# Kernel tuning notes

Measured on AMD Instinct MI355X. Metric: run time of the kernel, lower is better.

## Reference

```python
import jax, jax.numpy as jnp
import numpy as np

IMAGE_SIZE = 256
NEAR = 0.1
FAR = 100.0
EPS = 1e-3
BACKGROUND = jnp.array([0.0, 0.0, 0.0], dtype=jnp.float32)
CHUNK = 64  # faces processed per scan step (keeps [B,CHUNK,3,P] intermediate ~100MB)


def setup_inputs() -> dict:
    key = jax.random.key(0)
    k1, k2, k3, k4 = jax.random.split(key, 4)
    B, F, T = 2, 4096, 4
    # small triangles in NDC with z in (near, far)
    centers = jax.random.uniform(k1, (B, F, 1, 2), minval=-1.0, maxval=1.0)
    offsets = 0.15 * jax.random.normal(k2, (B, F, 3, 2))
    xy = centers + offsets
    z = jax.random.uniform(k3, (B, F, 1, 1), minval=1.0, maxval=20.0) \
        + 0.1 * jax.random.normal(k4, (B, F, 3, 1))
    faces = jnp.concatenate([xy, z], axis=-1).astype(jnp.float32)  # [B,F,3,3]
    textures = jax.random.uniform(jax.random.fold_in(key, 7), (B, F, T, T, T, 3),
                                  dtype=jnp.float32)
    return {"faces": faces, "textures": textures}


def _pixel_grid(is_):
    c = (2.0 * jnp.arange(is_, dtype=jnp.float32) + 1.0 - is_) / is_
    # kernel iterates rows top->bottom with y flipped (y up in NDC)
    yp, xp = jnp.meshgrid(-c, c, indexing="ij")  # [H,W]
    return xp.reshape(-1), yp.reshape(-1)  # [P]


def _raster_chunk(fchunk, xp, yp, near, far):
    # fchunk: [B,C,3verts,3coords]; xp,yp: [P]
    x = fchunk[..., 0]
    y = fchunk[..., 1]
    z = fchunk[..., 2]  # [B,C,3]
    x0, x1, x2 = x[..., 0:1], x[..., 1:2], x[..., 2:3]
    y0, y1, y2 = y[..., 0:1], y[..., 1:2], y[..., 2:3]

    # inside test: pixel on the CCW side of all 3 edges (back faces culled)
    def edge(ya, xa, yb, xb):
        return (yp - ya) * (xb - xa) - (xp - xa) * (yb - ya)  # [B,C,P]
    inside = (edge(y0, x0, y1, x1) >= 0) & (edge(y1, x1, y2, x2) >= 0) \
             & (edge(y2, x2, y0, x0) >= 0)

    # inverse of [[x0,y0,1],[x1,y1,1],[x2,y2,1]] via adjugate (as in CUDA kernel)
    x0s, x1s, x2s = x[..., 0], x[..., 1], x[..., 2]
    y0s, y1s, y2s = y[..., 0], y[..., 1], y[..., 2]
    det = x2s * (y0s - y1s) + x0s * (y1s - y2s) + x1s * (y2s - y0s)
    det = jnp.where(det >= 0, jnp.maximum(det, 1e-10), jnp.minimum(det, -1e-10))
    inv = jnp.stack([
        jnp.stack([y1s - y2s, x2s - x1s, x1s * y2s - x2s * y1s], -1),
        jnp.stack([y2s - y0s, x0s - x2s, x2s * y0s - x0s * y2s], -1),
        jnp.stack([y0s - y1s, x1s - x0s, x0s * y1s - x1s * y0s], -1),
    ], -2) / det[..., None, None]  # [B,C,3,3]

    # barycentric weights per pixel: [B,C,3,P]
    w = inv[..., 0, None] * xp + inv[..., 1, None] * yp + inv[..., 2, None]
    w = jnp.clip(w, 0.0, 1.0)
    w = w / jnp.maximum(w.sum(axis=2, keepdims=True), 1e-10)

    # perspective-correct depth: 1/zp = sum_k w_k / z_k
    inv_zp = (w / z[..., None]).sum(axis=2)  # [B,C,P]
    zp = 1.0 / jnp.maximum(inv_zp, 1e-10)
    valid = inside & (zp > near) & (zp < far)
    zp = jnp.where(valid, zp, far)
    return zp, jnp.moveaxis(w, 2, 3)  # zp:[B,C,P], w:[B,C,P,3]


def _rasterize_maps(faces, image_size, near, far):
    B, F = faces.shape[:2]
    P = image_size * image_size
    xp, yp = _pixel_grid(image_size)
    n_chunks = F // CHUNK
    fch = faces.reshape(B, n_chunks, CHUNK, 3, 3).transpose(1, 0, 2, 3, 4)
    ids = jnp.arange(F, dtype=jnp.int32).reshape(n_chunks, CHUNK)
    init = (jnp.full((B, P), far, jnp.float32),        # best depth (z-buffer)
            jnp.full((B, P), -1, jnp.int32),            # best face index
            jnp.zeros((B, P, 3), jnp.float32))          # best barycentric weights

    def step(carry, inp):
        bz, bf, bw = carry
        fchunk, idc = inp
        zp, w = _raster_chunk(fchunk, xp, yp, near, far)
        am = jnp.argmin(zp, axis=1)  # [B,P] nearest face within chunk
        zmin = jnp.take_along_axis(zp, am[:, None, :], axis=1)[:, 0]          # [B,P]
        wsel = jnp.take_along_axis(w, am[:, None, :, None], axis=1)[:, 0]     # [B,P,3]
        fsel = idc[am]                                                        # [B,P]
        upd = zmin < bz
        return (jnp.where(upd, zmin, bz),
                jnp.where(upd, fsel, bf),
                jnp.where(upd[..., None], wsel, bw)), None

    (bz, bf, bw), _ = jax.lax.scan(jax.checkpoint(step), init, (fch, ids))
    return bf, bw, bz  # face_index_map, weight_map, depth_map (flat pixels)


def _forward(faces, textures):
    B, F = faces.shape[:2]
    T = textures.shape[2]
    is_ = IMAGE_SIZE
    P = is_ * is_
    fidx, w, zp = _rasterize_maps(faces, is_, NEAR, FAR)
    mask = fidx >= 0
    fi = jnp.maximum(fidx, 0)

    # per-pixel vertex depths of hit face: [B,P,3]
    faces_z = faces[..., 2]
    fz = jax.vmap(lambda a, i: a[i])(faces_z, fi)

    # texture cube coords with perspective correction (as in CUDA kernel)
    tif = jnp.clip(w * (T - 1) * (zp[..., None] / fz), 0.0, T - 1 - EPS)
    lo = jnp.floor(tif).astype(jnp.int32)
    frac = tif - lo

    tex_flat = textures.reshape(B, F, T * T * T, 3)
    rgb = jnp.zeros((B, P, 3), jnp.float32)
    for pn in range(8):  # trilinear blend over 8 cube corners
        bits = [(pn >> k) & 1 for k in range(3)]
        idx = lo + jnp.array(bits, jnp.int32)
        wc = jnp.ones_like(frac[..., 0])
        for k in range(3):
            wc = wc * (frac[..., k] if bits[k] else (1.0 - frac[..., k]))
        lin = (idx[..., 0] * T + idx[..., 1]) * T + idx[..., 2]
        texel = jax.vmap(lambda tf, f, l: tf[f, l])(tex_flat, fi, lin)  # [B,P,3]
        rgb = rgb + wc[..., None] * texel

    rgb = jnp.where(mask[..., None], rgb, BACKGROUND)
    alpha = mask.astype(jnp.float32)
    return (rgb.reshape(B, is_, is_, 3),
            alpha.reshape(B, is_, is_),
            zp.reshape(B, is_, is_))


def reference(faces, textures):
    return _forward(faces, textures)
```

## Files before the change

### kernel.cpp

```cpp
#include <hip/hip_runtime.h>

#define IS 256
#define FNUM 4096
#define BATCH 2
#define NSPLIT 16
#define FSPLIT (FNUM / NSPLIT)
#define FAR_ 100.0f
#define NEAR_ 0.1f


__global__ __launch_bounds__(256, 8) void raster_kernel(
    const float* __restrict__ faces, unsigned int* __restrict__ keys)
{
#pragma clang fp contract(off)
  __shared__ float rec[256 * 12];
  __shared__ int cnt[4];

  const int tid = threadIdx.x;
  const int wid = tid >> 6, lane = tid & 63;
  const int z = blockIdx.z;
  const int b = z >> 4;
  const int split = z & 15;

  const int qx = tid & 15, qy = tid >> 4;
  const int col0 = blockIdx.x * 32 + qx * 2;
  const int row0 = blockIdx.y * 32 + qy * 2;

  const float xpA = (2.0f * (float)col0 + 1.0f - 256.0f) * (1.0f / 256.0f);
  const float xpB = (2.0f * (float)(col0 + 1) + 1.0f - 256.0f) * (1.0f / 256.0f);
  const float ypA = -((2.0f * (float)row0 + 1.0f - 256.0f) * (1.0f / 256.0f));
  const float ypB = -((2.0f * (float)(row0 + 1) + 1.0f - 256.0f) * (1.0f / 256.0f));

  const float txmin = (2.0f * (float)(blockIdx.x * 32) + 1.0f - 256.0f) * (1.0f / 256.0f) - 1e-3f;
  const float txmax = (2.0f * (float)(blockIdx.x * 32 + 31) + 1.0f - 256.0f) * (1.0f / 256.0f) + 1e-3f;
  const float tymax = -((2.0f * (float)(blockIdx.y * 32) + 1.0f - 256.0f) * (1.0f / 256.0f)) + 1e-3f;
  const float tymin = -((2.0f * (float)(blockIdx.y * 32 + 31) + 1.0f - 256.0f) * (1.0f / 256.0f)) - 1e-3f;

  const int f = split * FSPLIT + tid;
  const float* fp = faces + ((size_t)b * FNUM + f) * 9;
  const float x0 = fp[0], y0 = fp[1], z0 = fp[2];
  const float x1 = fp[3], y1 = fp[4], z1 = fp[5];
  const float x2 = fp[6], y2 = fp[7], z2 = fp[8];

  const float det = x2 * (y0 - y1) + x0 * (y1 - y2) + x1 * (y2 - y0);
  const float minx = fminf(fminf(x0, x1), x2), maxx = fmaxf(fmaxf(x0, x1), x2);
  const float miny = fminf(fminf(y0, y1), y2), maxy = fmaxf(fmaxf(y0, y1), y2);
  const bool keep = (det >= -1e-5f) &&
                    (minx <= txmax) && (maxx >= txmin) &&
                    (miny <= tymax) && (maxy >= tymin);

  const unsigned long long m = __ballot(keep);
  if (lane == 0) cnt[wid] = __popcll(m);
  __syncthreads();
  const int total = cnt[0] + cnt[1] + cnt[2] + cnt[3];
  if (keep) {
    int base = 0;
    for (int w = 0; w < wid; ++w) base += cnt[w];
    const int pos = base + __popcll(m & ((1ull << lane) - 1ull));
    const float cd = (det >= 0.0f) ? fmaxf(det, 1e-10f) : fminf(det, -1e-10f);
    const float rdet = __builtin_amdgcn_rcpf(cd);
    const float u0 = __builtin_amdgcn_rcpf(z0) * rdet;
    const float u1 = __builtin_amdgcn_rcpf(z1) * rdet;
    const float u2 = __builtin_amdgcn_rcpf(z2) * rdet;
    float4* r4 = (float4*)&rec[pos * 12];
    r4[0] = make_float4(x0, y0, x1, y1);
    r4[1] = make_float4(x2, y2, u0, u1);
    r4[2] = make_float4(u2, __int_as_float(f), 0.0f, 0.0f);
  }
  __syncthreads();

  unsigned int kAA = ~0u, kAB = ~0u, kBA = ~0u, kBB = ~0u;
  for (int i = 0; i < total; ++i) {
    const float4 r0 = ((const float4*)rec)[i * 3 + 0];
    const float4 r1 = ((const float4*)rec)[i * 3 + 1];
    const float4 r2 = ((const float4*)rec)[i * 3 + 2];
    const float fx0 = r0.x, fy0 = r0.y, fx1 = r0.z, fy1 = r0.w;
    const float fx2 = r1.x, fy2 = r1.y, u0 = r1.z, u1 = r1.w;
    const float u2 = r2.x;
    const unsigned int fid = (unsigned int)__float_as_int(r2.y);

    const float t01x = fx1 - fx0, t01y = fy1 - fy0;
    const float t12x = fx2 - fx1, t12y = fy2 - fy1;
    const float t20x = fx0 - fx2, t20y = fy0 - fy2;

    const float a01A = (ypA - fy0) * t01x, a01B = (ypB - fy0) * t01x;
    const float b01A = (xpA - fx0) * t01y, b01B = (xpB - fx0) * t01y;
    const float a12A = (ypA - fy1) * t12x, a12B = (ypB - fy1) * t12x;
    const float b12A = (xpA - fx1) * t12y, b12B = (xpB - fx1) * t12y;
    const float a20A = (ypA - fy2) * t20x, a20B = (ypB - fy2) * t20x;
    const float b20A = (xpA - fx2) * t20y, b20B = (xpB - fx2) * t20y;

#define PX(KK, AR, AC)                                                        \
    {                                                                         \
      const float e01 = a01##AR - b01##AC;                                    \
      const float e12 = a12##AR - b12##AC;                                    \
      const float e20 = a20##AR - b20##AC;                                    \
      const bool inside = fminf(fminf(e01, e12), e20) >= 0.0f;                \
      const float izp = fmaf(e12, u0, fmaf(e20, u1, e01 * u2));               \
      const float zp = __builtin_amdgcn_rcpf(izp);                            \
      const bool valid = inside && (izp > 0.01f) && (izp < 10.0f);            \
      const unsigned int key =                                                \
          valid ? ((__float_as_uint(zp) & 0xFFFFF000u) | fid) : ~0u;          \
      KK = (key < KK) ? key : KK;                                             \
    }
    PX(kAA, A, A) PX(kAB, A, B) PX(kBA, B, A) PX(kBB, B, B)
#undef PX
  }

  const int tbase = z * 65536 + ((int)blockIdx.y * 8 + (int)blockIdx.x) * 1024;
  const int ly = qy * 2, lx = qx * 2;
  keys[tbase + ly * 32 + lx]           = kAA;
  keys[tbase + ly * 32 + lx + 1]       = kAB;
  keys[tbase + (ly + 1) * 32 + lx]     = kBA;
  keys[tbase + (ly + 1) * 32 + lx + 1] = kBB;
}

__global__ __launch_bounds__(256) void resolve_kernel(
    const float* __restrict__ faces, const float* __restrict__ tex,
    const unsigned int* __restrict__ keys,
    float* __restrict__ out_rgb, float* __restrict__ out_alpha,
    float* __restrict__ out_z)
{
#pragma clang fp contract(off)
  const int p = blockIdx.x * 256 + threadIdx.x;
  const int b = p >> 16;
  const int pi = p & 65535;
  const int row = pi >> 8, col = pi & 255;
  const int tidx = ((row >> 5) * 8 + (col >> 5)) * 1024 + (row & 31) * 32 + (col & 31);

  unsigned int key = ~0u;
  for (int s = 0; s < NSPLIT; ++s) {
    const unsigned int k = keys[(b * NSPLIT + s) * 65536 + tidx];
    key = (k < key) ? k : key;
  }

  if (key == ~0u) {
    out_rgb[(size_t)p * 3 + 0] = 0.0f;
    out_rgb[(size_t)p * 3 + 1] = 0.0f;
    out_rgb[(size_t)p * 3 + 2] = 0.0f;
    out_alpha[p] = 0.0f;
    out_z[p] = FAR_;
    return;
  }

  const int fid = (int)(key & 0xFFFu);
  const float xp = (2.0f * (float)col + 1.0f - 256.0f) * (1.0f / 256.0f);
  const float yp = -((2.0f * (float)row + 1.0f - 256.0f) * (1.0f / 256.0f));

  const float* fp = faces + ((size_t)b * FNUM + fid) * 9;
  const float x0 = fp[0], y0 = fp[1], z0 = fp[2];
  const float x1 = fp[3], y1 = fp[4], z1 = fp[5];
  const float x2 = fp[6], y2 = fp[7], z2 = fp[8];

  const float det = x2 * (y0 - y1) + x0 * (y1 - y2) + x1 * (y2 - y0);
  const float cd = (det >= 0.0f) ? fmaxf(det, 1e-10f) : fminf(det, -1e-10f);
  const float rdet = __builtin_amdgcn_rcpf(cd);
  const float rz0 = __builtin_amdgcn_rcpf(z0);
  const float rz1 = __builtin_amdgcn_rcpf(z1);
  const float rz2 = __builtin_amdgcn_rcpf(z2);

  const float e01 = (yp - y0) * (x1 - x0) - (xp - x0) * (y1 - y0);
  const float e12 = (yp - y1) * (x2 - x1) - (xp - x1) * (y2 - y1);
  const float e20 = (yp - y2) * (x0 - x2) - (xp - x2) * (y0 - y2);

  float c0 = fminf(fmaxf(e12 * rdet, 0.0f), 1.0f);
  float c1 = fminf(fmaxf(e20 * rdet, 0.0f), 1.0f);
  float c2 = fminf(fmaxf(e01 * rdet, 0.0f), 1.0f);
  const float s = fmaxf((c0 + c1) + c2, 1e-10f);
  const float rs = __builtin_amdgcn_rcpf(s);
  const float w0 = c0 * rs, w1 = c1 * rs, w2 = c2 * rs;
  const float izp = (w0 * rz0 + w1 * rz1) + w2 * rz2;
  const float zp = __builtin_amdgcn_rcpf(fmaxf(izp, 1e-10f));

  const float t0 = fminf(fmaxf((w0 * 3.0f) * (zp * rz0), 0.0f), 2.999f);
  const float t1 = fminf(fmaxf((w1 * 3.0f) * (zp * rz1), 0.0f), 2.999f);
  const float t2 = fminf(fmaxf((w2 * 3.0f) * (zp * rz2), 0.0f), 2.999f);
  const float l0 = floorf(t0), l1 = floorf(t1), l2 = floorf(t2);
  const int i0 = (int)l0, i1 = (int)l1, i2 = (int)l2;
  const float fr0 = t0 - l0, fr1 = t1 - l1, fr2 = t2 - l2;

  const float* tb = tex + ((size_t)b * FNUM + fid) * 192;
  float rr = 0.f, rg = 0.f, rb = 0.f;
  for (int pn = 0; pn < 8; ++pn) {
    const int b0 = pn & 1, b1 = (pn >> 1) & 1, b2 = (pn >> 2) & 1;
    const float c0w = b0 ? fr0 : (1.0f - fr0);
    const float c1w = b1 ? fr1 : (1.0f - fr1);
    const float c2w = b2 ? fr2 : (1.0f - fr2);
    const float wc = (c0w * c1w) * c2w;
    const int lin = ((i0 + b0) * 4 + (i1 + b1)) * 4 + (i2 + b2);
    const float* tp = tb + lin * 3;
    rr = rr + wc * tp[0];
    rg = rg + wc * tp[1];
    rb = rb + wc * tp[2];
  }

  out_rgb[(size_t)p * 3 + 0] = rr;
  out_rgb[(size_t)p * 3 + 1] = rg;
  out_rgb[(size_t)p * 3 + 2] = rb;
  out_alpha[p] = 1.0f;
  out_z[p] = zp;
}

extern "C" void kernel_launch(void* const* d_in, const int* in_sizes, int n_in,
                              void* d_out, int out_size, void* d_ws, size_t ws_size,
                              hipStream_t stream) {
  const float* faces = (const float*)d_in[0];
  const float* tex   = (const float*)d_in[1];
  float* out = (float*)d_out;
  float* out_rgb   = out;
  float* out_alpha = out + 393216;
  float* out_z     = out + 393216 + 131072;

  unsigned int* keys = (unsigned int*)d_ws;

  dim3 gridA(IS / 32, IS / 32, BATCH * NSPLIT);
  hipLaunchKernelGGL(raster_kernel, gridA, dim3(256), 0, stream, faces, keys);

  dim3 gridC((BATCH * IS * IS) / 256, 1, 1);
  hipLaunchKernelGGL(resolve_kernel, gridC, dim3(256), 0, stream,
                     faces, tex, keys, out_rgb, out_alpha, out_z);
}
```

Measured before the change: 76.60 us.

## Merge split depth keys with atomicMin and vectorize resolve texture loads

The raster kernel now combines its per-split depth keys into one per-pixel buffer with atomicMin, skipping empty pixels. This replaces the 16 partial key buffers and the 16-way reduction in the resolve kernel, cutting global traffic substantially. The depth key is built from the bit-inverted inverse depth, which drops one reciprocal per pixel test. The resolve kernel also loads face data and pairs of texels as packed vectors and restructures the trilinear weights. The trade-offs are an extra memset on the stream and atomic contention, and the key quantization now applies to 1/z rather than z, which can change tie-breaking.

Result: no change. 75.50 us (-1.4%).

```diff
diff --git a/kernel.cpp b/kernel.cpp
--- a/kernel.cpp
+++ b/kernel.cpp
@@ -97,23 +97,24 @@
       const float e20 = a20##AR - b20##AC;                                    \
       const bool inside = fminf(fminf(e01, e12), e20) >= 0.0f;                \
       const float izp = fmaf(e12, u0, fmaf(e20, u1, e01 * u2));               \
-      const float zp = __builtin_amdgcn_rcpf(izp);                            \
       const bool valid = inside && (izp > 0.01f) && (izp < 10.0f);            \
       const unsigned int key =                                                \
-          valid ? ((__float_as_uint(zp) & 0xFFFFF000u) | fid) : ~0u;          \
+          valid ? ((~__float_as_uint(izp)) & 0xFFFFF000u) | fid : ~0u;        \
       KK = (key < KK) ? key : KK;                                             \
     }
     PX(kAA, A, A) PX(kAB, A, B) PX(kBA, B, A) PX(kBB, B, B)
 #undef PX
   }
 
-  const int tbase = z * 65536 + ((int)blockIdx.y * 8 + (int)blockIdx.x) * 1024;
-  const int ly = qy * 2, lx = qx * 2;
-  keys[tbase + ly * 32 + lx]           = kAA;
-  keys[tbase + ly * 32 + lx + 1]       = kAB;
-  keys[tbase + (ly + 1) * 32 + lx]     = kBA;
-  keys[tbase + (ly + 1) * 32 + lx + 1] = kBB;
+  const int pbase = b * 65536 + row0 * 256 + col0;
+  if (kAA != ~0u) atomicMin(&keys[pbase], kAA);
+  if (kAB != ~0u) atomicMin(&keys[pbase + 1], kAB);
+  if (kBA != ~0u) atomicMin(&keys[pbase + 256], kBA);
+  if (kBB != ~0u) atomicMin(&keys[pbase + 257], kBB);
 }
+
+struct __attribute__((packed, aligned(4))) F6 { float v[6]; };
+struct __attribute__((packed, aligned(4))) F9 { float v[9]; };
 
 __global__ __launch_bounds__(256) void resolve_kernel(
     const float* __restrict__ faces, const float* __restrict__ tex,
@@ -126,14 +127,8 @@
   const int b = p >> 16;
   const int pi = p & 65535;
   const int row = pi >> 8, col = pi & 255;
-  const int tidx = ((row >> 5) * 8 + (col >> 5)) * 1024 + (row & 31) * 32 + (col & 31);
-
-  unsigned int key = ~0u;
-  for (int s = 0; s < NSPLIT; ++s) {
-    const unsigned int k = keys[(b * NSPLIT + s) * 65536 + tidx];
-    key = (k < key) ? k : key;
-  }
-
+
+  const unsigned int key = keys[p];
   if (key == ~0u) {
     out_rgb[(size_t)p * 3 + 0] = 0.0f;
     out_rgb[(size_t)p * 3 + 1] = 0.0f;
@@ -147,10 +142,10 @@
   const float xp = (2.0f * (float)col + 1.0f - 256.0f) * (1.0f / 256.0f);
   const float yp = -((2.0f * (float)row + 1.0f - 256.0f) * (1.0f / 256.0f));
 
-  const float* fp = faces + ((size_t)b * FNUM + fid) * 9;
-  const float x0 = fp[0], y0 = fp[1], z0 = fp[2];
-  const float x1 = fp[3], y1 = fp[4], z1 = fp[5];
-  const float x2 = fp[6], y2 = fp[7], z2 = fp[8];
+  const F9 fdat = *(const F9*)(faces + ((size_t)b * FNUM + fid) * 9);
+  const float x0 = fdat.v[0], y0 = fdat.v[1], z0 = fdat.v[2];
+  const float x1 = fdat.v[3], y1 = fdat.v[4], z1 = fdat.v[5];
+  const float x2 = fdat.v[6], y2 = fdat.v[7], z2 = fdat.v[8];
 
   const float det = x2 * (y0 - y1) + x0 * (y1 - y2) + x1 * (y2 - y0);
   const float cd = (det >= 0.0f) ? fmaxf(det, 1e-10f) : fminf(det, -1e-10f);
@@ -178,20 +173,20 @@
   const float l0 = floorf(t0), l1 = floorf(t1), l2 = floorf(t2);
   const int i0 = (int)l0, i1 = (int)l1, i2 = (int)l2;
   const float fr0 = t0 - l0, fr1 = t1 - l1, fr2 = t2 - l2;
+  const float g0 = 1.0f - fr0, g1 = 1.0f - fr1, g2 = 1.0f - fr2;
 
   const float* tb = tex + ((size_t)b * FNUM + fid) * 192;
   float rr = 0.f, rg = 0.f, rb = 0.f;
-  for (int pn = 0; pn < 8; ++pn) {
-    const int b0 = pn & 1, b1 = (pn >> 1) & 1, b2 = (pn >> 2) & 1;
-    const float c0w = b0 ? fr0 : (1.0f - fr0);
-    const float c1w = b1 ? fr1 : (1.0f - fr1);
-    const float c2w = b2 ? fr2 : (1.0f - fr2);
-    const float wc = (c0w * c1w) * c2w;
-    const int lin = ((i0 + b0) * 4 + (i1 + b1)) * 4 + (i2 + b2);
-    const float* tp = tb + lin * 3;
-    rr = rr + wc * tp[0];
-    rg = rg + wc * tp[1];
-    rb = rb + wc * tp[2];
+#pragma unroll
+  for (int pn = 0; pn < 4; ++pn) {
+    const int b0 = pn & 1, b1 = (pn >> 1) & 1;
+    const float w01 = (b0 ? fr0 : g0) * (b1 ? fr1 : g1);
+    const float wz0 = w01 * g2, wz1 = w01 * fr2;
+    const int lin0 = ((i0 + b0) * 4 + (i1 + b1)) * 4 + i2;
+    const F6 t6 = *(const F6*)(tb + lin0 * 3);
+    rr = rr + wz0 * t6.v[0] + wz1 * t6.v[3];
+    rg = rg + wz0 * t6.v[1] + wz1 * t6.v[4];
+    rb = rb + wz0 * t6.v[2] + wz1 * t6.v[5];
   }
 
   out_rgb[(size_t)p * 3 + 0] = rr;
@@ -212,6 +207,7 @@
   float* out_z     = out + 393216 + 131072;
 
   unsigned int* keys = (unsigned int*)d_ws;
+  hipMemsetAsync(keys, 0xFF, (size_t)BATCH * IS * IS * sizeof(unsigned int), stream);
 
   dim3 gridA(IS / 32, IS / 32, BATCH * NSPLIT);
   hipLaunchKernelGGL(raster_kernel, gridA, dim3(256), 0, stream, faces, keys);
```
